# Performance work log

Hardware: AMD Instinct MI355X
Metric: run time of the kernel (lower is better)

## Reference

```python
import jax, jax.numpy as jnp
import numpy as np

B = 4            # batch size (max batch index + 1, fixed by construction)
H, W = 176, 200  # feature_map_size; x in [0,H), y in [0,W)
C_IN, C_OUT = 128, 256
BW, N = 4096, 64
EPS = 1e-5       # torch LayerNorm default


def setup_inputs() -> dict:
    key = jax.random.key(0)
    k1, k2, k3, k4, k5, k6, k7 = jax.random.split(key, 7)
    window_features = jax.random.normal(k1, (BW, N, C_IN), jnp.float32)
    bidx = jax.random.randint(k2, (BW, N, 1), 0, B)
    xidx = jax.random.randint(k3, (BW, N, 1), -8, H + 8)   # includes invalid coords
    yidx = jax.random.randint(k4, (BW, N, 1), -8, W + 8)
    window_indices = jnp.concatenate([bidx, xidx, yidx], axis=-1).astype(jnp.int32)
    norm_weight = 1.0 + 0.1 * jax.random.normal(k5, (C_IN,), jnp.float32)
    norm_bias = 0.1 * jax.random.normal(k6, (C_IN,), jnp.float32)
    lin_weight = jax.random.normal(k7, (C_OUT, C_IN), jnp.float32) / np.sqrt(C_IN)
    return {"window_features": window_features, "window_indices": window_indices,
            "norm_weight": norm_weight, "norm_bias": norm_bias, "lin_weight": lin_weight}


def reference(window_features, window_indices, norm_weight, norm_bias, lin_weight):
    # window_features: (BW, N, C_IN); window_indices: (BW, N, 3) = (batch, x, y)
    bw, n, c = window_features.shape
    feats = window_features.reshape(-1, c)                # (P, C)
    idx = window_indices.reshape(-1, 3)
    b, x, y = idx[:, 0], idx[:, 1], idx[:, 2]
    valid = (x >= 0) & (x < H) & (y >= 0) & (y < W)

    # unique + index_add_ + sparse-to-dense == scatter-add into dense BEV grid.
    # Invalid rows are routed out-of-bounds and dropped.
    bs = jnp.where(valid, b, B)
    xs = jnp.where(valid, x, 0)
    ys = jnp.where(valid, y, 0)
    # dense layout matches spconv: spatial_shape=[W, H], indices (b, y, x)
    dense_sum = jnp.zeros((B, W, H, c), window_features.dtype)
    dense_sum = dense_sum.at[bs, ys, xs].add(feats, mode="drop")
    count = jnp.zeros((B, W, H), window_features.dtype)
    count = count.at[bs, ys, xs].add(1.0, mode="drop")
    occupied = count > 0                                   # cells holding a unique voxel

    # LayerNorm over C (patch_norm=True) then Linear (bias=False) on occupied cells
    mu = jnp.mean(dense_sum, axis=-1, keepdims=True)
    var = jnp.mean(jnp.square(dense_sum - mu), axis=-1, keepdims=True)
    normed = (dense_sum - mu) * jax.lax.rsqrt(var + EPS) * norm_weight + norm_bias
    dense_out = jnp.einsum("bwhc,oc->bwho", normed, lin_weight)
    dense_out = jnp.where(occupied[..., None], dense_out, 0.0)  # empty cells stay zero

    # gather_operation: pull dense features back to each valid window point
    gathered = dense_out[jnp.where(valid, b, 0), ys, xs]   # (P, C_OUT)
    new_feats = jnp.where(valid[:, None], gathered, 0.0).reshape(bw, n, C_OUT)
    return new_feats, window_indices
```

## Files before the change

### kernel.cpp

```cpp
#include <hip/hip_runtime.h>
#include <stdint.h>

#define HH 176
#define WW 200
#define BB 4
#define CIN 128
#define COUT 256
#define NPTS (4096 * 64)
#define CELLS (BB * WW * HH)
#define FEAT_OUT_ELEMS ((size_t)NPTS * COUT)
#define CAP 32
#define BCELLS 16
#define LDSWN 132
#define LDSWO 260

typedef __attribute__((ext_vector_type(8))) short bf16x8;
typedef __attribute__((ext_vector_type(4))) float f32x4;

__device__ __forceinline__ unsigned short f2bf(float f) {
    union { float f; unsigned int u; } c; c.f = f;
    unsigned int u = c.u;
    u += 0x7fffu + ((u >> 16) & 1u);
    return (unsigned short)(u >> 16);
}
__device__ __forceinline__ float bf2f(unsigned int h16) {
    union { unsigned int u; float f; } c; c.u = h16 << 16;
    return c.f;
}

__global__ __launch_bounds__(256) void prep_kernel(
    const float* __restrict__ lw, unsigned short* __restrict__ wb,
    int* __restrict__ counts)
{
    int i = blockIdx.x * 256 + threadIdx.x;
    if (i < COUT * CIN) wb[i] = f2bf(lw[i]);
    counts[i] = 0;
}

__global__ __launch_bounds__(256) void build_kernel(
    const int* __restrict__ idx, int* __restrict__ counts, int* __restrict__ plist,
    float* __restrict__ out_idx, float* __restrict__ out_feats)
{
    __shared__ unsigned char validf[256];
    int tid = threadIdx.x;
    int p0 = blockIdx.x * 256;
    int p = p0 + tid;
    int b = idx[3 * p], x = idx[3 * p + 1], y = idx[3 * p + 2];
    out_idx[3 * p]     = (float)b;
    out_idx[3 * p + 1] = (float)x;
    out_idx[3 * p + 2] = (float)y;
    bool valid = ((unsigned)x < HH && (unsigned)y < WW);
    validf[tid] = valid ? 1 : 0;
    if (valid) {
        int cell = (b * WW + y) * HH + x;
        int slot = atomicAdd(&counts[cell], 1);
        if (slot < CAP) plist[(size_t)cell * CAP + slot] = p;
    }
    __syncthreads();
    int w = tid >> 6, lane = tid & 63;
    float4 z = { 0.0f, 0.0f, 0.0f, 0.0f };
    for (int v = w; v < 256; v += 4)
        if (!validf[v])
            *(float4*)(out_feats + (size_t)(p0 + v) * COUT + lane * 4) = z;
}

__global__ __launch_bounds__(256) void fused_kernel(
    const float* __restrict__ feats,
    const unsigned short* __restrict__ Wb,
    const int* __restrict__ counts,
    const int* __restrict__ plist,
    const float* __restrict__ nw, const float* __restrict__ nb,
    float* __restrict__ out)
{
    __shared__ unsigned short normedl[BCELLS * LDSWN];
    __shared__ unsigned short out16[BCELLS * LDSWO];

    int tid = threadIdx.x;
    int w = tid >> 6, lane = tid & 63;
    int l15 = lane & 15, g = lane >> 4;
    int kgrp = g * 8, orow = g * 4;
    int c0 = blockIdx.x * BCELLS;
    int cw0 = c0 + w * 4;

    float w0 = nw[lane * 2], w1 = nw[lane * 2 + 1];
    float b0 = nb[lane * 2], b1 = nb[lane * 2 + 1];

    int cnts[4];
    int4 pq[4];
    #pragma unroll
    for (int ci = 0; ci < 4; ++ci) {
        int n = counts[cw0 + ci];
        cnts[ci] = n < CAP ? n : CAP;
        pq[ci] = *(const int4*)(plist + (size_t)(cw0 + ci) * CAP);
    }

    #pragma unroll
    for (int ci = 0; ci < 4; ++ci) {
        int cnt = cnts[ci];
        float s0 = 0.0f, s1 = 0.0f;
        if (cnt > 0) { float2 t = *(const float2*)(feats + (size_t)pq[ci].x * CIN + lane * 2); s0 += t.x; s1 += t.y; }
        if (cnt > 1) { float2 t = *(const float2*)(feats + (size_t)pq[ci].y * CIN + lane * 2); s0 += t.x; s1 += t.y; }
        if (cnt > 2) { float2 t = *(const float2*)(feats + (size_t)pq[ci].z * CIN + lane * 2); s0 += t.x; s1 += t.y; }
        if (cnt > 3) { float2 t = *(const float2*)(feats + (size_t)pq[ci].w * CIN + lane * 2); s0 += t.x; s1 += t.y; }
        if (cnt > 4) {
            for (int s = 4; s < cnt; ++s) {
                int pid = plist[(size_t)(cw0 + ci) * CAP + s];
                float2 t = *(const float2*)(feats + (size_t)pid * CIN + lane * 2);
                s0 += t.x; s1 += t.y;
            }
        }
        float s = s0 + s1, ss = s0 * s0 + s1 * s1;
        #pragma unroll
        for (int m = 32; m >= 1; m >>= 1) {
            s  += __shfl_xor(s, m, 64);
            ss += __shfl_xor(ss, m, 64);
        }
        float mu  = s * (1.0f / 128.0f);
        float var = ss * (1.0f / 128.0f) - mu * mu;
        float inv = rsqrtf(var + 1e-5f);
        ushort2 st;
        st.x = f2bf((s0 - mu) * inv * w0 + b0);
        st.y = f2bf((s1 - mu) * inv * w1 + b1);
        *(ushort2*)(&normedl[(w * 4 + ci) * LDSWN + lane * 2]) = st;
    }
    __syncthreads();

    bf16x8 bfr[4];
    #pragma unroll
    for (int kk = 0; kk < 4; ++kk)
        bfr[kk] = *(const bf16x8*)(&normedl[l15 * LDSWN + kgrp + kk * 32]);

    #pragma unroll
    for (int i = 0; i < 4; ++i) {
        f32x4 acc = (f32x4){0.0f, 0.0f, 0.0f, 0.0f};
        #pragma unroll
        for (int kk = 0; kk < 4; ++kk) {
            bf16x8 av = *(const bf16x8*)(Wb + (size_t)((w * 64 + i * 16 + l15) * CIN) + kgrp + kk * 32);
            acc = __builtin_amdgcn_mfma_f32_16x16x32_bf16(av, bfr[kk], acc, 0, 0, 0);
        }
        ushort4 st;
        st.x = f2bf(acc[0]);
        st.y = f2bf(acc[1]);
        st.z = f2bf(acc[2]);
        st.w = f2bf(acc[3]);
        *(ushort4*)(&out16[l15 * LDSWO + w * 64 + i * 16 + orow]) = st;
    }
    __syncthreads();

    #pragma unroll
    for (int ci = 0; ci < 4; ++ci) {
        int cnt = cnts[ci];
        if (cnt > 0) {
            ushort4 v = *(const ushort4*)(&out16[(w * 4 + ci) * LDSWO + lane * 4]);
            float4 o4;
            o4.x = bf2f(v.x);
            o4.y = bf2f(v.y);
            o4.z = bf2f(v.z);
            o4.w = bf2f(v.w);
            *(float4*)(out + (size_t)pq[ci].x * COUT + lane * 4) = o4;
            if (cnt > 1) *(float4*)(out + (size_t)pq[ci].y * COUT + lane * 4) = o4;
            if (cnt > 2) *(float4*)(out + (size_t)pq[ci].z * COUT + lane * 4) = o4;
            if (cnt > 3) *(float4*)(out + (size_t)pq[ci].w * COUT + lane * 4) = o4;
            if (cnt > 4) {
                for (int s = 4; s < cnt; ++s) {
                    int pid = plist[(size_t)(cw0 + ci) * CAP + s];
                    *(float4*)(out + (size_t)pid * COUT + lane * 4) = o4;
                }
            }
        }
    }
}

extern "C" void kernel_launch(void* const* d_in, const int* in_sizes, int n_in,
                              void* d_out, int out_size, void* d_ws, size_t ws_size,
                              hipStream_t stream)
{
    const float* feats = (const float*)d_in[0];
    const int*   idx   = (const int*)d_in[1];
    const float* nw    = (const float*)d_in[2];
    const float* nb    = (const float*)d_in[3];
    const float* lw    = (const float*)d_in[4];
    float* out = (float*)d_out;

    char* ws = (char*)d_ws;
    int* counts = (int*)ws;
    int* plist  = (int*)(ws + (1u << 20));
    unsigned short* wb     = (unsigned short*)(ws + (20u << 20));

    prep_kernel<<<CELLS / 256, 256, 0, stream>>>(lw, wb, counts);
    build_kernel<<<NPTS / 256, 256, 0, stream>>>(idx, counts, plist, out + FEAT_OUT_ELEMS, out);
    fused_kernel<<<CELLS / BCELLS, 256, 0, stream>>>(feats, wb, counts, plist, nw, nb, out);
}
```

Measured before the change: 477.8 us.

## Split scatter-write into dense bf16 cell buffer plus coalesced per-point gather kernel

The fused kernel no longer scatters fp32 rows to each point. It writes its bf16 per-cell results into a dense workspace buffer, and a new writeout kernel gathers each point's row from that buffer in point order, writing zeros for invalid points. This replaces scattered random 1KB writes with sequential output writes plus random 512B reads. The cost is an extra kernel launch and a dense intermediate of about 72MB that is written in full, including empty cells.

Result: slower. 503.3 us (+5.3%).

```diff
diff --git a/kernel.cpp b/kernel.cpp
--- a/kernel.cpp
+++ b/kernel.cpp
@@ -38,39 +38,24 @@
 }
 
 __global__ __launch_bounds__(256) void build_kernel(
-    const int* __restrict__ idx, int* __restrict__ counts, int* __restrict__ plist,
-    float* __restrict__ out_idx, float* __restrict__ out_feats)
-{
-    __shared__ unsigned char validf[256];
-    int tid = threadIdx.x;
-    int p0 = blockIdx.x * 256;
-    int p = p0 + tid;
+    const int* __restrict__ idx, int* __restrict__ counts, int* __restrict__ plist)
+{
+    int p = blockIdx.x * 256 + threadIdx.x;
     int b = idx[3 * p], x = idx[3 * p + 1], y = idx[3 * p + 2];
-    out_idx[3 * p]     = (float)b;
-    out_idx[3 * p + 1] = (float)x;
-    out_idx[3 * p + 2] = (float)y;
-    bool valid = ((unsigned)x < HH && (unsigned)y < WW);
-    validf[tid] = valid ? 1 : 0;
-    if (valid) {
+    if ((unsigned)x < HH && (unsigned)y < WW) {
         int cell = (b * WW + y) * HH + x;
         int slot = atomicAdd(&counts[cell], 1);
         if (slot < CAP) plist[(size_t)cell * CAP + slot] = p;
     }
-    __syncthreads();
-    int w = tid >> 6, lane = tid & 63;
-    float4 z = { 0.0f, 0.0f, 0.0f, 0.0f };
-    for (int v = w; v < 256; v += 4)
-        if (!validf[v])
-            *(float4*)(out_feats + (size_t)(p0 + v) * COUT + lane * 4) = z;
-}
-
-__global__ __launch_bounds__(256) void fused_kernel(
+}
+
+__global__ __launch_bounds__(256) void cellgemm_kernel(
     const float* __restrict__ feats,
     const unsigned short* __restrict__ Wb,
     const int* __restrict__ counts,
     const int* __restrict__ plist,
     const float* __restrict__ nw, const float* __restrict__ nb,
-    float* __restrict__ out)
+    unsigned short* __restrict__ Cd)
 {
     __shared__ unsigned short normedl[BCELLS * LDSWN];
     __shared__ unsigned short out16[BCELLS * LDSWO];
@@ -148,27 +133,49 @@
     __syncthreads();
 
     #pragma unroll
-    for (int ci = 0; ci < 4; ++ci) {
-        int cnt = cnts[ci];
-        if (cnt > 0) {
-            ushort4 v = *(const ushort4*)(&out16[(w * 4 + ci) * LDSWO + lane * 4]);
-            float4 o4;
-            o4.x = bf2f(v.x);
-            o4.y = bf2f(v.y);
-            o4.z = bf2f(v.z);
-            o4.w = bf2f(v.w);
-            *(float4*)(out + (size_t)pq[ci].x * COUT + lane * 4) = o4;
-            if (cnt > 1) *(float4*)(out + (size_t)pq[ci].y * COUT + lane * 4) = o4;
-            if (cnt > 2) *(float4*)(out + (size_t)pq[ci].z * COUT + lane * 4) = o4;
-            if (cnt > 3) *(float4*)(out + (size_t)pq[ci].w * COUT + lane * 4) = o4;
-            if (cnt > 4) {
-                for (int s = 4; s < cnt; ++s) {
-                    int pid = plist[(size_t)(cw0 + ci) * CAP + s];
-                    *(float4*)(out + (size_t)pid * COUT + lane * 4) = o4;
-                }
-            }
-        }
-    }
+    for (int r = 0; r < 4; ++r) {
+        int e = r * 256 + tid;
+        int c = e >> 6;
+        int q = e & 63;
+        *(ushort4*)(Cd + (size_t)(c0 + c) * COUT + q * 4) =
+            *(const ushort4*)(&out16[c * LDSWO + q * 4]);
+    }
+}
+
+__global__ __launch_bounds__(256) void writeout_kernel(
+    const unsigned short* __restrict__ Cd, const int* __restrict__ idx,
+    float* __restrict__ out_feats, float* __restrict__ out_idx)
+{
+    int tid = threadIdx.x;
+    int w = tid >> 6, lane = tid & 63;
+    int pbase = blockIdx.x * 8;
+
+    if (tid < 24) out_idx[(size_t)pbase * 3 + tid] = (float)idx[pbase * 3 + tid];
+
+    int pA = pbase + w * 2, pB = pA + 1;
+    int bA = idx[3 * pA], xA = idx[3 * pA + 1], yA = idx[3 * pA + 2];
+    int bB = idx[3 * pB], xB = idx[3 * pB + 1], yB = idx[3 * pB + 2];
+    bool vA = ((unsigned)xA < HH && (unsigned)yA < WW);
+    bool vB = ((unsigned)xB < HH && (unsigned)yB < WW);
+
+    uint2 dA = {0u, 0u}, dB = {0u, 0u};
+    if (vA) {
+        size_t cA = ((size_t)bA * WW + yA) * HH + xA;
+        dA = *(const uint2*)(Cd + cA * COUT + lane * 4);
+    }
+    if (vB) {
+        size_t cB = ((size_t)bB * WW + yB) * HH + xB;
+        dB = *(const uint2*)(Cd + cB * COUT + lane * 4);
+    }
+
+    float4 oA, oB;
+    oA.x = bf2f(dA.x & 0xffffu); oA.y = bf2f(dA.x >> 16);
+    oA.z = bf2f(dA.y & 0xffffu); oA.w = bf2f(dA.y >> 16);
+    oB.x = bf2f(dB.x & 0xffffu); oB.y = bf2f(dB.x >> 16);
+    oB.z = bf2f(dB.y & 0xffffu); oB.w = bf2f(dB.y >> 16);
+
+    *(float4*)(out_feats + (size_t)pA * COUT + lane * 4) = oA;
+    *(float4*)(out_feats + (size_t)pB * COUT + lane * 4) = oB;
 }
 
 extern "C" void kernel_launch(void* const* d_in, const int* in_sizes, int n_in,
@@ -185,9 +192,11 @@
     char* ws = (char*)d_ws;
     int* counts = (int*)ws;
     int* plist  = (int*)(ws + (1u << 20));
-    unsigned short* wb     = (unsigned short*)(ws + (20u << 20));
+    unsigned short* wb = (unsigned short*)(ws + (20u << 20));
+    unsigned short* Cd = (unsigned short*)(ws + (21u << 20));
 
     prep_kernel<<<CELLS / 256, 256, 0, stream>>>(lw, wb, counts);
-    build_kernel<<<NPTS / 256, 256, 0, stream>>>(idx, counts, plist, out + FEAT_OUT_ELEMS, out);
-    fused_kernel<<<CELLS / BCELLS, 256, 0, stream>>>(feats, wb, counts, plist, nw, nb, out);
-}
+    build_kernel<<<NPTS / 256, 256, 0, stream>>>(idx, counts, plist);
+    cellgemm_kernel<<<CELLS / BCELLS, 256, 0, stream>>>(feats, wb, counts, plist, nw, nb, Cd);
+    writeout_kernel<<<NPTS / 8, 256, 0, stream>>>(Cd, idx, out, out + FEAT_OUT_ELEMS);
+}
```
